# Performance work log

Hardware: AMD Instinct MI355X
Metric: run time of the kernel (lower is better)

The kernel has to match this reference:

```python
import jax, jax.numpy as jnp
import numpy as np

N_A = 100000   # target-type nodes
N_B = 100000   # source-type nodes
IN_DIM = 256
OUT_DIM = 256
E = 320000     # edges per meta-path
LN_EPS = 1e-5


def setup_inputs() -> dict:
    key = jax.random.key(0)
    ks = jax.random.split(key, 10)
    w_scale = 1.0 / np.sqrt(IN_DIM)
    return {
        "x_A": jax.random.normal(ks[0], (N_A, IN_DIM), jnp.float32),
        "x_B": jax.random.normal(ks[1], (N_B, IN_DIM), jnp.float32),
        "edge_index0": jax.random.randint(ks[2], (2, E), 0, N_A, dtype=jnp.int32),
        "edge_index1": jax.random.randint(ks[3], (2, E), 0, N_A, dtype=jnp.int32),
        "W0": jax.random.normal(ks[4], (IN_DIM, OUT_DIM), jnp.float32) * w_scale,
        "b0": jnp.zeros((OUT_DIM,), jnp.float32),
        "W1": jax.random.normal(ks[5], (IN_DIM, OUT_DIM), jnp.float32) * w_scale,
        "b1": jnp.zeros((OUT_DIM,), jnp.float32),
        "sem_vec": jax.random.normal(ks[6], (OUT_DIM,), jnp.float32),
        "gamma": jnp.ones((OUT_DIM,), jnp.float32),
        "beta": jnp.zeros((OUT_DIM,), jnp.float32),
    }


def _layer_norm(x, gamma, beta):
    mu = jnp.mean(x, axis=-1, keepdims=True)
    var = jnp.mean((x - mu) ** 2, axis=-1, keepdims=True)
    return (x - mu) * jax.lax.rsqrt(var + LN_EPS) * gamma + beta


def _path_mean_agg(x_src, W, b, ei, n_dst):
    # project ALL source nodes first (matches torch: proj_src = Linear(src_x))
    proj = x_src @ W + b                      # (N_src, OUT)
    msgs = proj[ei[0]]                        # gather  (E, OUT)
    agg = jax.ops.segment_sum(msgs, ei[1], num_segments=n_dst)   # scatter_add
    cnt = jax.ops.segment_sum(jnp.ones((ei.shape[1],), proj.dtype), ei[1],
                              num_segments=n_dst)
    return agg / jnp.clip(cnt, 1.0)[:, None]  # count-normalized mean


def reference(x_A, x_B, edge_index0, edge_index1, W0, b0, W1, b1,
              sem_vec, gamma, beta):
    n_dst = x_A.shape[0]
    agg0 = _path_mean_agg(x_B, W0, b0, edge_index0, n_dst)
    agg1 = _path_mean_agg(x_B, W1, b1, edge_index1, n_dst)
    stack = jnp.stack([agg0, agg1], axis=0)               # (P=2, N_A, OUT)
    scores = jnp.einsum('pnd,d->pn', jnp.tanh(stack), sem_vec)
    weights = jax.nn.softmax(scores, axis=0)              # over meta-paths
    fused = jnp.sum(stack * weights[..., None], axis=0)   # (N_A, OUT)
    out_A = _layer_norm(jax.nn.relu(fused), gamma, beta)
    out_B = jnp.zeros((x_B.shape[0], OUT_DIM), x_B.dtype)  # no path targets B
    return out_A, out_B
```

## Files before the change

kernel.cpp:

```cpp
#include <hip/hip_runtime.h>
#include <math.h>

#define NA 100000
#define NB 100000
#define KDIM 256
#define ODIM 256
#define NEDGE 320000
#define NCAT 512
#define NBUCK (2 * NA)
#define NPART 782

typedef unsigned int u32;
typedef __bf16 bf16x8 __attribute__((ext_vector_type(8)));
typedef float  f32x4  __attribute__((ext_vector_type(4)));

__global__ __launch_bounds__(256) void convert_w(
    const float* __restrict__ W0, const float* __restrict__ b0,
    const float* __restrict__ W1, const float* __restrict__ b1,
    __bf16* __restrict__ Wth, __bf16* __restrict__ Wtl,
    float* __restrict__ bcat)
{
    const int t = blockIdx.x * 256 + threadIdx.x;
    if (t >= 512 * 32) return;
    const int n  = t >> 5;
    const int kb = (t & 31) * 8;
    const float* src = (n < ODIM) ? (W0 + n) : (W1 + (n - ODIM));
    bf16x8 vh, vl;
    #pragma unroll
    for (int j = 0; j < 8; ++j) {
        float w = src[(size_t)(kb + j) * ODIM];
        __bf16 h = (__bf16)w;
        vh[j] = h;
        vl[j] = (__bf16)(w - (float)h);
    }
    *(bf16x8*)&Wth[(size_t)n * KDIM + kb] = vh;
    *(bf16x8*)&Wtl[(size_t)n * KDIM + kb] = vl;
    if ((t & 31) == 0) bcat[n] = (n < ODIM) ? b0[n] : b1[n - ODIM];
}

__global__ __launch_bounds__(256) void proj_gemm(
    const float* __restrict__ x,
    const __bf16* __restrict__ Wth, const __bf16* __restrict__ Wtl,
    const float* __restrict__ bcat, float* __restrict__ projf)
{
    __shared__ __align__(16) char smem[32768];
    bf16x8* Ah = (bf16x8*)smem;
    bf16x8* Al = (bf16x8*)(smem + 8192);
    bf16x8* Bh = (bf16x8*)(smem + 16384);
    bf16x8* Bl = (bf16x8*)(smem + 24576);

    const int t    = threadIdx.x;
    const int w    = t >> 6;
    const int lane = t & 63;
    const int m0   = blockIdx.y * 128;
    const int n0   = blockIdx.x * 128;
    const int wm   = w & 1, wn = w >> 1;

    const int srow = w * 16 + (lane & 15);
    const int kc   = (lane >> 4) * 8;
    const int arow0 = min(m0 + srow,      NB - 1);
    const int arow1 = min(m0 + srow + 64, NB - 1);
    const int brow0 = n0 + srow;
    const int brow1 = brow0 + 64;

    f32x4 acc[4][4] = {};

    for (int k0 = 0; k0 < KDIM; k0 += 32) {
        const float4* pa0 = (const float4*)&x[(size_t)arow0 * KDIM + k0 + kc];
        const float4* pa1 = (const float4*)&x[(size_t)arow1 * KDIM + k0 + kc];
        float4 a00 = pa0[0], a01 = pa0[1];
        float4 a10 = pa1[0], a11 = pa1[1];
        bf16x8 ah0, al0, ah1, al1;
        {
            float f0[8] = {a00.x, a00.y, a00.z, a00.w, a01.x, a01.y, a01.z, a01.w};
            float f1[8] = {a10.x, a10.y, a10.z, a10.w, a11.x, a11.y, a11.z, a11.w};
            #pragma unroll
            for (int j = 0; j < 8; ++j) {
                __bf16 h0 = (__bf16)f0[j];
                ah0[j] = h0; al0[j] = (__bf16)(f0[j] - (float)h0);
                __bf16 h1 = (__bf16)f1[j];
                ah1[j] = h1; al1[j] = (__bf16)(f1[j] - (float)h1);
            }
        }
        bf16x8 gh0 = *(const bf16x8*)&Wth[(size_t)brow0 * KDIM + k0 + kc];
        bf16x8 gh1 = *(const bf16x8*)&Wth[(size_t)brow1 * KDIM + k0 + kc];
        bf16x8 gl0 = *(const bf16x8*)&Wtl[(size_t)brow0 * KDIM + k0 + kc];
        bf16x8 gl1 = *(const bf16x8*)&Wtl[(size_t)brow1 * KDIM + k0 + kc];

        __syncthreads();
        Ah[t] = ah0;  Ah[t + 256] = ah1;
        Al[t] = al0;  Al[t + 256] = al1;
        Bh[t] = gh0;  Bh[t + 256] = gh1;
        Bl[t] = gl0;  Bl[t + 256] = gl1;
        __syncthreads();

        bf16x8 afh[4], afl[4], bgh[4], bgl[4];
        #pragma unroll
        for (int i = 0; i < 4; ++i) {
            afh[i] = Ah[(wm * 4 + i) * 64 + lane];
            afl[i] = Al[(wm * 4 + i) * 64 + lane];
        }
        #pragma unroll
        for (int j = 0; j < 4; ++j) {
            bgh[j] = Bh[(wn * 4 + j) * 64 + lane];
            bgl[j] = Bl[(wn * 4 + j) * 64 + lane];
        }
        #pragma unroll
        for (int i = 0; i < 4; ++i)
            #pragma unroll
            for (int j = 0; j < 4; ++j) {
                acc[i][j] = __builtin_amdgcn_mfma_f32_16x16x32_bf16(
                    afl[i], bgh[j], acc[i][j], 0, 0, 0);
                acc[i][j] = __builtin_amdgcn_mfma_f32_16x16x32_bf16(
                    afh[i], bgl[j], acc[i][j], 0, 0, 0);
                acc[i][j] = __builtin_amdgcn_mfma_f32_16x16x32_bf16(
                    afh[i], bgh[j], acc[i][j], 0, 0, 0);
            }
    }

    float bias[4];
    #pragma unroll
    for (int j = 0; j < 4; ++j)
        bias[j] = bcat[n0 + wn * 64 + j * 16 + (lane & 15)];

    __syncthreads();
    float* ep = (float*)(smem + w * 4352);
    const int quad = lane >> 4, c16 = lane & 15;
    const int lr = lane >> 2, lc = (lane & 3) * 16;

    for (int i = 0; i < 4; ++i) {
        #pragma unroll
        for (int j = 0; j < 4; ++j)
            #pragma unroll
            for (int r = 0; r < 4; ++r)
                ep[(quad * 4 + r) * 68 + j * 16 + c16] = acc[i][j][r] + bias[j];
        __syncthreads();
        f32x4 v0 = *(f32x4*)&ep[lr * 68 + lc + 0];
        f32x4 v1 = *(f32x4*)&ep[lr * 68 + lc + 4];
        f32x4 v2 = *(f32x4*)&ep[lr * 68 + lc + 8];
        f32x4 v3 = *(f32x4*)&ep[lr * 68 + lc + 12];
        __syncthreads();
        const int rg = m0 + wm * 64 + i * 16 + lr;
        if (rg < NB) {
            float* dst = &projf[(size_t)rg * NCAT + n0 + wn * 64 + lc];
            *(f32x4*)(dst + 0)  = v0;
            *(f32x4*)(dst + 4)  = v1;
            *(f32x4*)(dst + 8)  = v2;
            *(f32x4*)(dst + 12) = v3;
        }
    }
}

__global__ __launch_bounds__(256) void csr_count(
    const int* __restrict__ ei0, const int* __restrict__ ei1,
    u32* __restrict__ cnt)
{
    const int gid = blockIdx.x * 256 + threadIdx.x;
    if (gid >= 2 * NEDGE) return;
    const int p = (gid >= NEDGE) ? 1 : 0;
    const int j = gid - p * NEDGE;
    const int* ei = p ? ei1 : ei0;
    const int dst = ei[NEDGE + j];
    atomicAdd(&cnt[p * NA + dst], 1u);
}

__global__ __launch_bounds__(256) void scan1(
    const u32* __restrict__ cnt, u32* __restrict__ offs, u32* __restrict__ parts)
{
    __shared__ u32 s[256];
    const int t = threadIdx.x;
    const int idx = blockIdx.x * 256 + t;
    u32 v = (idx < NBUCK) ? cnt[idx] : 0u;
    s[t] = v;
    __syncthreads();
    #pragma unroll
    for (int off = 1; off < 256; off <<= 1) {
        u32 u = (t >= off) ? s[t - off] : 0u;
        __syncthreads();
        s[t] += u;
        __syncthreads();
    }
    if (idx < NBUCK) offs[idx] = s[t] - v;
    if (t == 255) parts[blockIdx.x] = s[255];
}

__global__ __launch_bounds__(1024) void scan2(u32* __restrict__ parts)
{
    __shared__ u32 s[1024];
    const int t = threadIdx.x;
    u32 v = (t < NPART) ? parts[t] : 0u;
    s[t] = v;
    __syncthreads();
    #pragma unroll
    for (int off = 1; off < 1024; off <<= 1) {
        u32 u = (t >= off) ? s[t - off] : 0u;
        __syncthreads();
        s[t] += u;
        __syncthreads();
    }
    if (t < NPART) parts[t] = s[t] - v;
}

__global__ __launch_bounds__(256) void scan3(
    u32* __restrict__ offs, const u32* __restrict__ parts, u32* __restrict__ cursor)
{
    const int idx = blockIdx.x * 256 + threadIdx.x;
    if (idx < NBUCK) {
        u32 o = offs[idx] + parts[blockIdx.x];
        offs[idx] = o;
        cursor[idx] = o;
    }
    if (idx == 0) offs[NBUCK] = 2 * NEDGE;
}

__global__ __launch_bounds__(256) void csr_fill(
    const int* __restrict__ ei0, const int* __restrict__ ei1,
    u32* __restrict__ cursor, int* __restrict__ elist)
{
    const int gid = blockIdx.x * 256 + threadIdx.x;
    if (gid >= 2 * NEDGE) return;
    const int p = (gid >= NEDGE) ? 1 : 0;
    const int j = gid - p * NEDGE;
    const int* ei = p ? ei1 : ei0;
    const int src = ei[j];
    const int dst = ei[NEDGE + j];
    const u32 pos = atomicAdd(&cursor[p * NA + dst], 1u);
    elist[pos] = src;
}

__global__ __launch_bounds__(256) void gather_finalize(
    const float* __restrict__ projf,
    const u32* __restrict__ offs, const int* __restrict__ elist,
    float* __restrict__ out,
    const float* __restrict__ sem, const float* __restrict__ gamma,
    const float* __restrict__ beta)
{
    const int row  = (int)((blockIdx.x * (size_t)blockDim.x + threadIdx.x) >> 6);
    const int lane = threadIdx.x & 63;
    if (row >= NA) return;
    const int p  = lane >> 5;
    const int li = lane & 31;
    const int c  = li * 8;

    const u32 bs = offs[p * NA + row];
    const u32 be = offs[p * NA + row + 1];

    float a[8] = {};
    for (u32 j = bs; j < be; ++j) {
        const int src = elist[j];
        const float4* rp = (const float4*)&projf[(size_t)src * NCAT + p * ODIM + c];
        float4 v0 = rp[0], v1 = rp[1];
        a[0] += v0.x; a[1] += v0.y; a[2] += v0.z; a[3] += v0.w;
        a[4] += v1.x; a[5] += v1.y; a[6] += v1.z; a[7] += v1.w;
    }
    const float inv = 1.0f / fmaxf((float)(be - bs), 1.0f);
    float m[8];
    #pragma unroll
    for (int i = 0; i < 8; ++i) m[i] = a[i] * inv;

    float4 s0 = *(const float4*)&sem[c];
    float4 s1 = *(const float4*)&sem[c + 4];
    float sv[8] = {s0.x, s0.y, s0.z, s0.w, s1.x, s1.y, s1.z, s1.w};
    float s = 0.f;
    #pragma unroll
    for (int i = 0; i < 8; ++i) s += tanhf(m[i]) * sv[i];
    #pragma unroll
    for (int off = 1; off <= 16; off <<= 1) s += __shfl_xor(s, off);
    const float so = __shfl_xor(s, 32);
    const float mx = fmaxf(s, so);
    const float e  = __expf(s - mx), eo = __expf(so - mx);
    const float wown = e / (e + eo), woth = eo / (e + eo);

    float fused[8];
    float sum = 0.f, sq = 0.f;
    #pragma unroll
    for (int i = 0; i < 8; ++i) {
        const float mo = __shfl_xor(m[i], 32);
        float f = fmaxf(wown * m[i] + woth * mo, 0.f);
        fused[i] = f;
        sum += f;
        sq  += f * f;
    }
    #pragma unroll
    for (int off = 1; off <= 32; off <<= 1) {
        sum += __shfl_xor(sum, off);
        sq  += __shfl_xor(sq,  off);
    }
    const float mu  = sum * (0.5f / ODIM);
    const float var = sq  * (0.5f / ODIM) - mu * mu;
    const float rinv = rsqrtf(var + 1e-5f);

    if (p == 0) {
        float4 g0 = *(const float4*)&gamma[c];
        float4 g1 = *(const float4*)&gamma[c + 4];
        float4 b0 = *(const float4*)&beta[c];
        float4 b1 = *(const float4*)&beta[c + 4];
        float gv[8] = {g0.x, g0.y, g0.z, g0.w, g1.x, g1.y, g1.z, g1.w};
        float bv[8] = {b0.x, b0.y, b0.z, b0.w, b1.x, b1.y, b1.z, b1.w};
        float o[8];
        #pragma unroll
        for (int i = 0; i < 8; ++i) o[i] = (fused[i] - mu) * rinv * gv[i] + bv[i];
        float4 o0, o1;
        o0.x = o[0]; o0.y = o[1]; o0.z = o[2]; o0.w = o[3];
        o1.x = o[4]; o1.y = o[5]; o1.z = o[6]; o1.w = o[7];
        *(float4*)&out[(size_t)row * ODIM + c]     = o0;
        *(float4*)&out[(size_t)row * ODIM + c + 4] = o1;
    }
}

extern "C" void kernel_launch(void* const* d_in, const int* in_sizes, int n_in,
                              void* d_out, int out_size, void* d_ws, size_t ws_size,
                              hipStream_t stream)
{
    const float* xB   = (const float*)d_in[1];
    const int*   ei0  = (const int*)d_in[2];
    const int*   ei1  = (const int*)d_in[3];
    const float* W0   = (const float*)d_in[4];
    const float* b0   = (const float*)d_in[5];
    const float* W1   = (const float*)d_in[6];
    const float* b1   = (const float*)d_in[7];
    const float* sem  = (const float*)d_in[8];
    const float* gam  = (const float*)d_in[9];
    const float* bet  = (const float*)d_in[10];

    float* out = (float*)d_out;

    float* projf = (float*)d_ws;

    u32* cnt    = (u32*)(out + (size_t)NA * ODIM);
    u32* offs   = cnt    + 200064;
    u32* parts  = offs   + 200128;
    u32* cursor = parts  + 1024;
    int* elist  = (int*)(cursor + 200064);
    __bf16* Wth = (__bf16*)(elist + 640000);
    __bf16* Wtl = Wth + (size_t)512 * KDIM;
    float*  bcat = (float*)(Wtl + (size_t)512 * KDIM);

    convert_w<<<64, 256, 0, stream>>>(W0, b0, W1, b1, Wth, Wtl, bcat);

    dim3 ggrid(NCAT / 128, (NB + 127) / 128);
    proj_gemm<<<ggrid, 256, 0, stream>>>(xB, Wth, Wtl, bcat, projf);

    hipMemsetAsync(cnt, 0, (size_t)NBUCK * sizeof(u32), stream);
    const int egrid = (2 * NEDGE + 255) / 256;
    csr_count<<<egrid, 256, 0, stream>>>(ei0, ei1, cnt);
    scan1<<<NPART, 256, 0, stream>>>(cnt, offs, parts);
    scan2<<<1, 1024, 0, stream>>>(parts);
    scan3<<<NPART, 256, 0, stream>>>(offs, parts, cursor);
    csr_fill<<<egrid, 256, 0, stream>>>(ei0, ei1, cursor, elist);

    gather_finalize<<<(NA + 3) / 4, 256, 0, stream>>>(projf, offs, elist, out,
                                                      sem, gam, bet);

    hipMemsetAsync(out + (size_t)NA * ODIM, 0,
                   (size_t)NA * ODIM * sizeof(float), stream);
}
```

Measured before the change: 670.0 us.

## Store projections in fp16 and load GEMM operands directly into registers

The projection GEMM now loads A and B fragments straight from global memory into registers instead of staging them through shared memory, which removes the per-k-step barriers and LDS traffic but means each element is loaded by several waves. The projection output buffer is stored as fp16 instead of fp32, halving the bytes written by the GEMM and read by the gather-aggregation kernel. The fp16 storage lowers the precision of the intermediate projections, which could affect accuracy tolerance.

```diff
diff --git a/kernel.cpp b/kernel.cpp
--- a/kernel.cpp
+++ b/kernel.cpp
@@ -11,8 +11,9 @@
 #define NPART 782
 
 typedef unsigned int u32;
-typedef __bf16 bf16x8 __attribute__((ext_vector_type(8)));
-typedef float  f32x4  __attribute__((ext_vector_type(4)));
+typedef __bf16    bf16x8 __attribute__((ext_vector_type(8)));
+typedef _Float16  f16x8  __attribute__((ext_vector_type(8)));
+typedef float     f32x4  __attribute__((ext_vector_type(4)));
 
 __global__ __launch_bounds__(256) void convert_w(
     const float* __restrict__ W0, const float* __restrict__ b0,
@@ -41,13 +42,9 @@
 __global__ __launch_bounds__(256) void proj_gemm(
     const float* __restrict__ x,
     const __bf16* __restrict__ Wth, const __bf16* __restrict__ Wtl,
-    const float* __restrict__ bcat, float* __restrict__ projf)
-{
-    __shared__ __align__(16) char smem[32768];
-    bf16x8* Ah = (bf16x8*)smem;
-    bf16x8* Al = (bf16x8*)(smem + 8192);
-    bf16x8* Bh = (bf16x8*)(smem + 16384);
-    bf16x8* Bl = (bf16x8*)(smem + 24576);
+    const float* __restrict__ bcat, _Float16* __restrict__ projf)
+{
+    __shared__ float ep[4][16][68];
 
     const int t    = threadIdx.x;
     const int w    = t >> 6;
@@ -55,98 +52,90 @@
     const int m0   = blockIdx.y * 128;
     const int n0   = blockIdx.x * 128;
     const int wm   = w & 1, wn = w >> 1;
-
-    const int srow = w * 16 + (lane & 15);
+    const int r16  = lane & 15;
     const int kc   = (lane >> 4) * 8;
-    const int arow0 = min(m0 + srow,      NB - 1);
-    const int arow1 = min(m0 + srow + 64, NB - 1);
-    const int brow0 = n0 + srow;
-    const int brow1 = brow0 + 64;
+
+    size_t aoff[4];
+    size_t bhoff[4];
+    #pragma unroll
+    for (int i = 0; i < 4; ++i) {
+        const int ar = min(m0 + wm * 64 + i * 16 + r16, NB - 1);
+        aoff[i] = (size_t)ar * KDIM + kc;
+    }
+    #pragma unroll
+    for (int j = 0; j < 4; ++j) {
+        const int br = n0 + wn * 64 + j * 16 + r16;
+        bhoff[j] = (size_t)br * KDIM + kc;
+    }
 
     f32x4 acc[4][4] = {};
 
     for (int k0 = 0; k0 < KDIM; k0 += 32) {
-        const float4* pa0 = (const float4*)&x[(size_t)arow0 * KDIM + k0 + kc];
-        const float4* pa1 = (const float4*)&x[(size_t)arow1 * KDIM + k0 + kc];
-        float4 a00 = pa0[0], a01 = pa0[1];
-        float4 a10 = pa1[0], a11 = pa1[1];
-        bf16x8 ah0, al0, ah1, al1;
-        {
-            float f0[8] = {a00.x, a00.y, a00.z, a00.w, a01.x, a01.y, a01.z, a01.w};
-            float f1[8] = {a10.x, a10.y, a10.z, a10.w, a11.x, a11.y, a11.z, a11.w};
+        bf16x8 ah[4], al[4], bh[4], bl[4];
+        #pragma unroll
+        for (int i = 0; i < 4; ++i) {
+            const float4* pa = (const float4*)&x[aoff[i] + k0];
+            float4 v0 = pa[0], v1 = pa[1];
+            float f[8] = {v0.x, v0.y, v0.z, v0.w, v1.x, v1.y, v1.z, v1.w};
             #pragma unroll
-            for (int j = 0; j < 8; ++j) {
-                __bf16 h0 = (__bf16)f0[j];
-                ah0[j] = h0; al0[j] = (__bf16)(f0[j] - (float)h0);
-                __bf16 h1 = (__bf16)f1[j];
-                ah1[j] = h1; al1[j] = (__bf16)(f1[j] - (float)h1);
+            for (int e = 0; e < 8; ++e) {
+                __bf16 h = (__bf16)f[e];
+                ah[i][e] = h;
+                al[i][e] = (__bf16)(f[e] - (float)h);
             }
         }
-        bf16x8 gh0 = *(const bf16x8*)&Wth[(size_t)brow0 * KDIM + k0 + kc];
-        bf16x8 gh1 = *(const bf16x8*)&Wth[(size_t)brow1 * KDIM + k0 + kc];
-        bf16x8 gl0 = *(const bf16x8*)&Wtl[(size_t)brow0 * KDIM + k0 + kc];
-        bf16x8 gl1 = *(const bf16x8*)&Wtl[(size_t)brow1 * KDIM + k0 + kc];
-
-        __syncthreads();
-        Ah[t] = ah0;  Ah[t + 256] = ah1;
-        Al[t] = al0;  Al[t + 256] = al1;
-        Bh[t] = gh0;  Bh[t + 256] = gh1;
-        Bl[t] = gl0;  Bl[t + 256] = gl1;
-        __syncthreads();
-
-        bf16x8 afh[4], afl[4], bgh[4], bgl[4];
-        #pragma unroll
-        for (int i = 0; i < 4; ++i) {
-            afh[i] = Ah[(wm * 4 + i) * 64 + lane];
-            afl[i] = Al[(wm * 4 + i) * 64 + lane];
-        }
         #pragma unroll
         for (int j = 0; j < 4; ++j) {
-            bgh[j] = Bh[(wn * 4 + j) * 64 + lane];
-            bgl[j] = Bl[(wn * 4 + j) * 64 + lane];
+            bh[j] = *(const bf16x8*)&Wth[bhoff[j] + k0];
+            bl[j] = *(const bf16x8*)&Wtl[bhoff[j] + k0];
         }
         #pragma unroll
         for (int i = 0; i < 4; ++i)
             #pragma unroll
             for (int j = 0; j < 4; ++j) {
                 acc[i][j] = __builtin_amdgcn_mfma_f32_16x16x32_bf16(
-                    afl[i], bgh[j], acc[i][j], 0, 0, 0);
+                    al[i], bh[j], acc[i][j], 0, 0, 0);
                 acc[i][j] = __builtin_amdgcn_mfma_f32_16x16x32_bf16(
-                    afh[i], bgl[j], acc[i][j], 0, 0, 0);
+                    ah[i], bl[j], acc[i][j], 0, 0, 0);
                 acc[i][j] = __builtin_amdgcn_mfma_f32_16x16x32_bf16(
-                    afh[i], bgh[j], acc[i][j], 0, 0, 0);
+                    ah[i], bh[j], acc[i][j], 0, 0, 0);
             }
     }
 
     float bias[4];
     #pragma unroll
     for (int j = 0; j < 4; ++j)
-        bias[j] = bcat[n0 + wn * 64 + j * 16 + (lane & 15)];
-
-    __syncthreads();
-    float* ep = (float*)(smem + w * 4352);
+        bias[j] = bcat[n0 + wn * 64 + j * 16 + r16];
+
     const int quad = lane >> 4, c16 = lane & 15;
     const int lr = lane >> 2, lc = (lane & 3) * 16;
 
     for (int i = 0; i < 4; ++i) {
+        __syncthreads();
         #pragma unroll
         for (int j = 0; j < 4; ++j)
             #pragma unroll
             for (int r = 0; r < 4; ++r)
-                ep[(quad * 4 + r) * 68 + j * 16 + c16] = acc[i][j][r] + bias[j];
-        __syncthreads();
-        f32x4 v0 = *(f32x4*)&ep[lr * 68 + lc + 0];
-        f32x4 v1 = *(f32x4*)&ep[lr * 68 + lc + 4];
-        f32x4 v2 = *(f32x4*)&ep[lr * 68 + lc + 8];
-        f32x4 v3 = *(f32x4*)&ep[lr * 68 + lc + 12];
-        __syncthreads();
+                ep[w][quad * 4 + r][j * 16 + c16] = acc[i][j][r] + bias[j];
+        __syncthreads();
+        f32x4 v0 = *(f32x4*)&ep[w][lr][lc + 0];
+        f32x4 v1 = *(f32x4*)&ep[w][lr][lc + 4];
+        f32x4 v2 = *(f32x4*)&ep[w][lr][lc + 8];
+        f32x4 v3 = *(f32x4*)&ep[w][lr][lc + 12];
         const int rg = m0 + wm * 64 + i * 16 + lr;
         if (rg < NB) {
-            float* dst = &projf[(size_t)rg * NCAT + n0 + wn * 64 + lc];
-            *(f32x4*)(dst + 0)  = v0;
-            *(f32x4*)(dst + 4)  = v1;
-            *(f32x4*)(dst + 8)  = v2;
-            *(f32x4*)(dst + 12) = v3;
+            f16x8 o0, o1;
+            o0[0] = (_Float16)v0[0]; o0[1] = (_Float16)v0[1];
+            o0[2] = (_Float16)v0[2]; o0[3] = (_Float16)v0[3];
+            o0[4] = (_Float16)v1[0]; o0[5] = (_Float16)v1[1];
+            o0[6] = (_Float16)v1[2]; o0[7] = (_Float16)v1[3];
+            o1[0] = (_Float16)v2[0]; o1[1] = (_Float16)v2[1];
+            o1[2] = (_Float16)v2[2]; o1[3] = (_Float16)v2[3];
+            o1[4] = (_Float16)v3[0]; o1[5] = (_Float16)v3[1];
+            o1[6] = (_Float16)v3[2]; o1[7] = (_Float16)v3[3];
+            _Float16* dst = &projf[(size_t)rg * NCAT + n0 + wn * 64 + lc];
+            *(f16x8*)(dst + 0) = o0;
+            *(f16x8*)(dst + 8) = o1;
         }
     }
 }
@@ -229,7 +218,7 @@
 }
 
 __global__ __launch_bounds__(256) void gather_finalize(
-    const float* __restrict__ projf,
+    const _Float16* __restrict__ projf,
     const u32* __restrict__ offs, const int* __restrict__ elist,
     float* __restrict__ out,
     const float* __restrict__ sem, const float* __restrict__ gamma,
@@ -248,10 +237,9 @@
     float a[8] = {};
     for (u32 j = bs; j < be; ++j) {
         const int src = elist[j];
-        const float4* rp = (const float4*)&projf[(size_t)src * NCAT + p * ODIM + c];
-        float4 v0 = rp[0], v1 = rp[1];
-        a[0] += v0.x; a[1] += v0.y; a[2] += v0.z; a[3] += v0.w;
-        a[4] += v1.x; a[5] += v1.y; a[6] += v1.z; a[7] += v1.w;
+        const f16x8 v = *(const f16x8*)&projf[(size_t)src * NCAT + p * ODIM + c];
+        #pragma unroll
+        for (int i = 0; i < 8; ++i) a[i] += (float)v[i];
     }
     const float inv = 1.0f / fmaxf((float)(be - bs), 1.0f);
     float m[8];
@@ -325,7 +313,7 @@
 
     float* out = (float*)d_out;
 
-    float* projf = (float*)d_ws;
+    _Float16* projf = (_Float16*)d_ws;
 
     u32* cnt    = (u32*)(out + (size_t)NA * ODIM);
     u32* offs   = cnt    + 200064;
```

Result: slower. 693.2 us (+3.5%).
